# Kernel tuning notes

Hardware: AMD Instinct MI355X
Metric: run time of the kernel (lower is better)

Reference implementation:

```python
import jax, jax.numpy as jnp
import numpy as np

M = 256      # max_child_num
H = 256      # hidden_size
F = 256      # node feature_size (== H, required by original view())
T = 4        # edge_type_num
ITERS = 2    # num_dec_gnn_iterations
NSEM = 40    # Tree.num_sem


def setup_inputs() -> dict:
    key = jax.random.key(0)
    ks = jax.random.split(key, 18)

    def w(k, shape):
        fan_in = shape[-2] if len(shape) >= 2 else shape[-1]
        return jax.random.normal(k, shape, jnp.float32) / np.sqrt(fan_in)

    return {
        "parent_feature": jax.random.normal(ks[0], (1, F), jnp.float32),
        # mlp_parent: F -> H*M
        "W_parent": w(ks[1], (F, H * M)), "b_parent": jnp.zeros((H * M,), jnp.float32),
        # mlp_exists: H -> 1
        "W_exists": w(ks[2], (H, 1)), "b_exists": jnp.zeros((1,), jnp.float32),
        # mlp_edge_latent: 2H -> H
        "W_el": w(ks[3], (2 * H, H)), "b_el": jnp.zeros((H,), jnp.float32),
        # mlp_edge_exists[t]: H -> 1, stacked over T
        "W_ee": w(ks[4], (T, H)), "b_ee": jnp.zeros((T,), jnp.float32),
        # node_edge_op[i]: (3H + T) -> H, stacked over ITERS
        "W_ne": w(ks[5], (ITERS, 3 * H + T, H)), "b_ne": jnp.zeros((ITERS, H), jnp.float32),
        # mlp_child: H*(ITERS+1) -> H
        "W_child": w(ks[6], (H * (ITERS + 1), H)), "b_child": jnp.zeros((H,), jnp.float32),
        # mlp_sem: H -> NSEM
        "W_sem": w(ks[7], (H, NSEM)), "b_sem": jnp.zeros((NSEM,), jnp.float32),
        # mlp_child2: H -> F
        "W_child2": w(ks[8], (H, F)), "b_child2": jnp.zeros((F,), jnp.float32),
    }


def _forward(parent_feature, W_parent, b_parent, W_exists, b_exists,
             W_el, b_el, W_ee, b_ee, W_ne, b_ne,
             W_child, b_child, W_sem, b_sem, W_child2, b_child2):
    # parent -> per-child latent feats [M, H]
    pf = jax.nn.relu(parent_feature @ W_parent + b_parent)   # [1, M*H]
    child_feats = pf.reshape(M, H)

    child_exists_logits = child_feats @ W_exists + b_exists  # [M, 1]

    # pairwise edge latents [M, M, H]: relu(Linear(cat(feat_i, feat_j)))
    # split the 2H x H weight to avoid materializing the [M, M, 2H] concat
    W_el_i, W_el_j = W_el[:H], W_el[H:]
    edge_latents = jax.nn.relu(
        (child_feats @ W_el_i)[:, None, :] + (child_feats @ W_el_j)[None, :, :] + b_el
    )  # [M, M, H]

    # per-type edge existence logits [M, M, T]
    edge_exists_logits = jnp.einsum('mnh,th->mnt', edge_latents, W_ee) + b_ee

    # dynamic edge set (torch.nonzero) expressed as a dense mask over (i, j, t):
    # edge exists iff its logit > 0 and both endpoint nodes exist
    node_exists = child_exists_logits[:, 0] > 0                      # [M]
    edge_mask = (edge_exists_logits > 0) \
        & node_exists[:, None, None] & node_exists[None, :, None]    # [M, M, T]
    has_edge = jnp.any(edge_mask)

    cf = child_feats
    iter_feats = [cf]
    for i in range(ITERS):
        # node_edge_op input is cat([feat_i, feat_j, edge_latent, type_logit]);
        # split the (3H+T) x H weight into blocks to avoid the big concat.
        Wi, Wj = W_ne[i, :H], W_ne[i, H:2 * H]
        We, Wt = W_ne[i, 2 * H:3 * H], W_ne[i, 3 * H:]
        # type_logit is one-hot(t) * edge_exists_logits[i,j,t], so its matmul
        # contribution is logits[m,n,t] * Wt[t]
        pre = ((cf @ Wi)[:, None, None, :]
               + (cf @ Wj)[None, :, None, :]
               + jnp.einsum('mnh,hk->mnk', edge_latents, We)[:, :, None, :]
               + edge_exists_logits[..., None] * Wt[None, None, :, :]
               + b_ne[i])                                            # [M, M, T, H]
        msg = jax.nn.relu(pre)
        msg = jnp.where(edge_mask[..., None], msg, 0.0)
        # scatter_max over source node with zero-initialized out; msgs >= 0 so
        # masked-zero + max reproduces torch_scatter.scatter_max exactly
        new_cf = jnp.max(msg, axis=(1, 2))                           # [M, H]
        cf = jnp.where(has_edge, new_cf, cf)  # torch skips update if no edges
        iter_feats.append(cf)

    feats_cat = jnp.concatenate(iter_feats, axis=1)                  # [M, H*(ITERS+1)]
    hidden = jax.nn.relu(feats_cat @ W_child + b_child)              # [M, H]
    child_sem_logits = (hidden @ W_sem + b_sem).reshape(1, M, NSEM)
    out_child_feats = jax.nn.relu(hidden @ W_child2 + b_child2).reshape(1, M, F)
    return (out_child_feats,
            child_sem_logits,
            child_exists_logits.reshape(1, M, 1),
            edge_exists_logits.reshape(1, M, M, T))


def reference(parent_feature, W_parent, b_parent, W_exists, b_exists,
              W_el, b_el, W_ee, b_ee, W_ne, b_ne,
              W_child, b_child, W_sem, b_sem, W_child2, b_child2):
    return _forward(parent_feature, W_parent, b_parent, W_exists, b_exists,
                    W_el, b_el, W_ee, b_ee, W_ne, b_ne,
                    W_child, b_child, W_sem, b_sem, W_child2, b_child2)
```

## Files before the change

kernel.cpp:

```cpp
#include <hip/hip_runtime.h>
#include <hip/hip_bf16.h>

#define MMH 256
#define TT 4
#define NSEMN 40
#define HM 65536

using short8 = __attribute__((ext_vector_type(8))) short;
using f32x4  = __attribute__((ext_vector_type(4))) float;

__device__ __forceinline__ unsigned short f2bf(float x) {
  union { float f; unsigned int u; } v; v.f = x;
  unsigned int r = v.u + 0x7fffu + ((v.u >> 16) & 1u);
  return (unsigned short)(r >> 16);
}

__global__ __launch_bounds__(256) void k_parent(
    const float* __restrict__ pf, const float* __restrict__ Wp,
    const float* __restrict__ bp, float* __restrict__ cat) {
  int j = blockIdx.x * 256 + threadIdx.x;
  float acc = bp[j];
  #pragma unroll 8
  for (int f = 0; f < MMH; ++f) acc += pf[f] * Wp[(size_t)f * HM + j];
  int m = j >> 8, h = j & 255;
  cat[m * 768 + h] = fmaxf(acc, 0.0f);
}

__global__ __launch_bounds__(64) void k_cel(
    const float* __restrict__ cat, const float* __restrict__ Wex,
    const float* __restrict__ bex, float* __restrict__ cel,
    float* __restrict__ out_ex, int* __restrict__ flags) {
  int m = blockIdx.x, l = threadIdx.x;
  float s = 0.f;
  for (int h = l; h < MMH; h += 64) s += cat[m * 768 + h] * Wex[h];
  #pragma unroll
  for (int off = 32; off > 0; off >>= 1) s += __shfl_down(s, off);
  if (l == 0) { float v = s + bex[0]; cel[m] = v; out_ex[m] = v; }
  if (m == 0 && l == 0) flags[0] = 0;
}

__global__ __launch_bounds__(256) void k_gemm16(
    const float* __restrict__ A, int lda,
    const float* __restrict__ B0, const float* __restrict__ B1, int ldb,
    const float* __restrict__ bias,
    float* __restrict__ C0, float* __restrict__ C1, int ldc,
    int N2, int K2, int relu) {
  const float* B = blockIdx.z ? B1 : B0;
  float*       C = blockIdx.z ? C1 : C0;
  __shared__ float As[16][17], Bs[16][17];
  int tx = threadIdx.x, ty = threadIdx.y;
  int row = blockIdx.y * 16 + ty, col = blockIdx.x * 16 + tx;
  float acc = 0.f;
  for (int k0 = 0; k0 < K2; k0 += 16) {
    As[ty][tx] = A[row * lda + k0 + tx];
    Bs[ty][tx] = (col < N2) ? B[(k0 + ty) * ldb + col] : 0.f;
    __syncthreads();
    #pragma unroll
    for (int kk = 0; kk < 16; ++kk) acc += As[ty][kk] * Bs[kk][tx];
    __syncthreads();
  }
  if (col < N2) {
    if (bias) acc += bias[col];
    if (relu) acc = fmaxf(acc, 0.f);
    C[row * ldc + col] = acc;
  }
}

__global__ __launch_bounds__(256) void k_tr(
    const float* __restrict__ Wne, const float* __restrict__ Wee,
    unsigned short* __restrict__ WeTb, float* __restrict__ Wee4g) {
  int i = blockIdx.z;
  const float* We = Wne + (size_t)(i * 772 + 512) * 256;
  unsigned short* out = WeTb + i * 65536;
  __shared__ float t[32][33];
  int tx = threadIdx.x, ty = threadIdx.y;
  int h0 = blockIdx.y * 32, k0 = blockIdx.x * 32;
  #pragma unroll
  for (int j = 0; j < 4; ++j)
    t[ty + j * 8][tx] = We[(size_t)(h0 + ty + j * 8) * 256 + k0 + tx];
  __syncthreads();
  #pragma unroll
  for (int j = 0; j < 4; ++j) {
    int kl = ty + j * 8;
    out[((h0 >> 5) * 256 + k0 + kl) * 32 + tx] = f2bf(t[tx][kl]);
  }
  if (blockIdx.x == 0 && blockIdx.y == 0 && i == 0) {
    int t2 = ty * 32 + tx;
    float4 w;
    w.x = Wee[t2]; w.y = Wee[256 + t2]; w.z = Wee[512 + t2]; w.w = Wee[768 + t2];
    ((float4*)Wee4g)[t2] = w;
  }
}

#define XP 260
__global__ __launch_bounds__(256) void k_edge(
    const float* __restrict__ Xi, const float* __restrict__ Xj,
    const float* __restrict__ bel, const float* __restrict__ Wee4g,
    const float* __restrict__ bee, const float* __restrict__ cel,
    float* __restrict__ out_eel, int* __restrict__ flags) {
  __shared__ float XiS[16 * XP], XjS[16 * XP];
  __shared__ int anyEdge;
  int tid = threadIdx.x;
  int m0 = (blockIdx.x >> 4) * 16, n0 = (blockIdx.x & 15) * 16;
  if (tid == 0) anyEdge = 0;
  #pragma unroll
  for (int j = 0; j < 4; ++j) {
    int c = tid + 256 * j;
    int row = c >> 6, c4 = (c & 63) * 4;
    float4 v = *(const float4*)(Xi + (m0 + row) * 256 + c4);
    float4 b = *(const float4*)(bel + c4);
    v.x += b.x; v.y += b.y; v.z += b.z; v.w += b.w;
    *(float4*)&XiS[row * XP + c4] = v;
    *(float4*)&XjS[row * XP + c4] = *(const float4*)(Xj + (n0 + row) * 256 + c4);
  }
  __syncthreads();
  int tm = tid >> 4, tn = tid & 15;
  const float* xr = &XiS[tm * XP];
  const float* yr = &XjS[tn * XP];
  float4 s = {0.f, 0.f, 0.f, 0.f};
  for (int h = 0; h < 256; h += 8) {
    float4 a0 = *(const float4*)&xr[h], a1 = *(const float4*)&xr[h + 4];
    float4 b0 = *(const float4*)&yr[h], b1 = *(const float4*)&yr[h + 4];
    float e[8];
    e[0] = fmaxf(a0.x + b0.x, 0.f); e[1] = fmaxf(a0.y + b0.y, 0.f);
    e[2] = fmaxf(a0.z + b0.z, 0.f); e[3] = fmaxf(a0.w + b0.w, 0.f);
    e[4] = fmaxf(a1.x + b1.x, 0.f); e[5] = fmaxf(a1.y + b1.y, 0.f);
    e[6] = fmaxf(a1.z + b1.z, 0.f); e[7] = fmaxf(a1.w + b1.w, 0.f);
    #pragma unroll
    for (int q = 0; q < 8; ++q) {
      float4 w = ((const float4*)Wee4g)[h + q];
      s.x += e[q] * w.x; s.y += e[q] * w.y;
      s.z += e[q] * w.z; s.w += e[q] * w.w;
    }
  }
  int m = m0 + tm, n = n0 + tn;
  s.x += bee[0]; s.y += bee[1]; s.z += bee[2]; s.w += bee[3];
  ((float4*)out_eel)[m * 256 + n] = s;
  bool edge = (cel[m] > 0.f) && (cel[n] > 0.f) &&
              (s.x > 0.f || s.y > 0.f || s.z > 0.f || s.w > 0.f);
  if (__ballot(edge) != 0ull && (tid & 63) == 0) atomicOr(&anyEdge, 1);
  __syncthreads();
  if (tid == 0 && anyEdge) atomicOr(flags, 1);
}

__global__ __launch_bounds__(256) void k_zero(float* __restrict__ p) {
  p[blockIdx.x * 256 + threadIdx.x] = 0.f;
}

#define ELP 56
__global__ __launch_bounds__(256) void k_iter(
    const float* __restrict__ Xi, const float* __restrict__ Xj,
    const float* __restrict__ bel, const unsigned short* __restrict__ WeTb,
    const float* __restrict__ Ai, const float* __restrict__ Bj,
    const float* __restrict__ Wt, const float* __restrict__ bne,
    const float* __restrict__ eel, const float* __restrict__ cel,
    float* __restrict__ newcf) {
  __shared__ unsigned short ELs[64 * ELP];
  __shared__ unsigned short WesT[256 * ELP];
  int tid = threadIdx.x;
  int w = tid >> 6, lane = tid & 63;
  int m0 = (blockIdx.x >> 4) * 4, n0 = (blockIdx.x & 15) * 16;
  f32x4 acc[4][4] = {};

  for (int h0 = 0; h0 < MMH; h0 += 32) {
    {
      int row = tid & 63, g = tid >> 6;
      int mI = m0 + (row >> 4), nI = n0 + (row & 15);
      const float4* xip = (const float4*)(Xi + mI * MMH + h0 + g * 8);
      const float4* xjp = (const float4*)(Xj + nI * MMH + h0 + g * 8);
      const float4* bp  = (const float4*)(bel + h0 + g * 8);
      float4 x0 = xip[0], x1 = xip[1];
      float4 y0 = xjp[0], y1 = xjp[1];
      float4 c0 = bp[0],  c1 = bp[1];
      short8 v;
      v[0] = (short)f2bf(fmaxf(x0.x + y0.x + c0.x, 0.f));
      v[1] = (short)f2bf(fmaxf(x0.y + y0.y + c0.y, 0.f));
      v[2] = (short)f2bf(fmaxf(x0.z + y0.z + c0.z, 0.f));
      v[3] = (short)f2bf(fmaxf(x0.w + y0.w + c0.w, 0.f));
      v[4] = (short)f2bf(fmaxf(x1.x + y1.x + c1.x, 0.f));
      v[5] = (short)f2bf(fmaxf(x1.y + y1.y + c1.y, 0.f));
      v[6] = (short)f2bf(fmaxf(x1.z + y1.z + c1.z, 0.f));
      v[7] = (short)f2bf(fmaxf(x1.w + y1.w + c1.w, 0.f));
      *(short8*)&ELs[row * ELP + g * 8] = v;
    }
    {
      const unsigned short* WeT = WeTb + (h0 >> 5) * 8192;
      #pragma unroll
      for (int j = 0; j < 4; ++j) {
        int g = tid + 256 * j;
        short8 v = *(const short8*)(WeT + g * 8);
        *(short8*)&WesT[(g >> 2) * ELP + (g & 3) * 8] = v;
      }
    }
    __syncthreads();
    short8 af[4], bf[4];
    #pragma unroll
    for (int rt = 0; rt < 4; ++rt)
      af[rt] = *(const short8*)&ELs[(rt * 16 + (lane & 15)) * ELP + (lane >> 4) * 8];
    #pragma unroll
    for (int ct = 0; ct < 4; ++ct)
      bf[ct] = *(const short8*)&WesT[(w * 64 + ct * 16 + (lane & 15)) * ELP + (lane >> 4) * 8];
    #pragma unroll
    for (int rt = 0; rt < 4; ++rt)
      #pragma unroll
      for (int ct = 0; ct < 4; ++ct)
        acc[rt][ct] = __builtin_amdgcn_mfma_f32_16x16x32_bf16(af[rt], bf[ct], acc[rt][ct], 0, 0, 0);
    __syncthreads();
  }

  int col = lane & 15, grp = lane >> 4;
  #pragma unroll
  for (int rt = 0; rt < 4; ++rt) {
    int m = m0 + rt;
    bool nem = cel[m] > 0.f;
    float4 e4[4]; bool nen[4];
    #pragma unroll
    for (int r = 0; r < 4; ++r) {
      int n = n0 + grp * 4 + r;
      e4[r] = ((const float4*)eel)[m * 256 + n];
      nen[r] = cel[n] > 0.f;
    }
    #pragma unroll
    for (int ct = 0; ct < 4; ++ct) {
      int k = w * 64 + ct * 16 + col;
      float basek = Ai[m * MMH + k] + bne[k];
      float wt0 = Wt[0 * MMH + k], wt1 = Wt[1 * MMH + k];
      float wt2 = Wt[2 * MMH + k], wt3 = Wt[3 * MMH + k];
      float vmax = 0.f;
      #pragma unroll
      for (int r = 0; r < 4; ++r) {
        int n = n0 + grp * 4 + r;
        float base = acc[rt][ct][r] + basek + Bj[n * MMH + k];
        if (nem && nen[r]) {
          if (e4[r].x > 0.f) vmax = fmaxf(vmax, base + e4[r].x * wt0);
          if (e4[r].y > 0.f) vmax = fmaxf(vmax, base + e4[r].y * wt1);
          if (e4[r].z > 0.f) vmax = fmaxf(vmax, base + e4[r].z * wt2);
          if (e4[r].w > 0.f) vmax = fmaxf(vmax, base + e4[r].w * wt3);
        }
      }
      vmax = fmaxf(vmax, __shfl_xor(vmax, 16));
      vmax = fmaxf(vmax, __shfl_xor(vmax, 32));
      if (grp == 0 && vmax > 0.f)
        atomicMax((unsigned int*)&newcf[m * MMH + k], __float_as_uint(vmax));
    }
  }
}

__global__ __launch_bounds__(256) void k_select(
    const int* __restrict__ flags, float* __restrict__ newcf,
    float* __restrict__ cat, int iter) {
  int idx = blockIdx.x * 256 + threadIdx.x;
  int m = idx >> 8, k = idx & 255;
  float prev = cat[m * 768 + iter * 256 + k];
  float v = flags[0] ? newcf[idx] : prev;
  cat[m * 768 + (iter + 1) * 256 + k] = v;
  newcf[idx] = 0.f;
}

extern "C" void kernel_launch(void* const* d_in, const int* in_sizes, int n_in,
                              void* d_out, int out_size, void* d_ws, size_t ws_size,
                              hipStream_t stream) {
  const float* pf   = (const float*)d_in[0];
  const float* Wp   = (const float*)d_in[1];
  const float* bp   = (const float*)d_in[2];
  const float* Wex  = (const float*)d_in[3];
  const float* bex  = (const float*)d_in[4];
  const float* Wel  = (const float*)d_in[5];
  const float* bel  = (const float*)d_in[6];
  const float* Wee  = (const float*)d_in[7];
  const float* bee  = (const float*)d_in[8];
  const float* Wne  = (const float*)d_in[9];
  const float* bne  = (const float*)d_in[10];
  const float* Wch  = (const float*)d_in[11];
  const float* bch  = (const float*)d_in[12];
  const float* Wsem = (const float*)d_in[13];
  const float* bsem = (const float*)d_in[14];
  const float* Wch2 = (const float*)d_in[15];
  const float* bch2 = (const float*)d_in[16];
  float* out = (float*)d_out;
  float* ws  = (float*)d_ws;

  float* cat    = ws;
  float* Xi     = ws + 196608;
  float* Xj     = Xi + 65536;
  float* Ai     = Xj + 65536;
  float* Bj     = Ai + 65536;
  float* newcf  = Bj + 65536;
  float* hidden = newcf + 65536;
  float* cel    = hidden + 65536;
  int*   flags  = (int*)(cel + 256);
  float* Wee4g  = cel + 512;
  unsigned short* WeTb = (unsigned short*)(Wee4g + 1024);

  float* out_cf  = out;
  float* out_sem = out + 65536;
  float* out_ex  = out + 75776;
  float* out_eel = out + 76032;

  dim3 b16(16, 16);
  k_parent<<<256, 256, 0, stream>>>(pf, Wp, bp, cat);
  k_cel<<<256, 64, 0, stream>>>(cat, Wex, bex, cel, out_ex, flags);
  k_tr<<<dim3(8, 8, 2), dim3(32, 8), 0, stream>>>(Wne, Wee, WeTb, Wee4g);
  k_gemm16<<<dim3(16, 16, 2), b16, 0, stream>>>(cat, 768, Wel, Wel + 65536, 256,
                                                nullptr, Xi, Xj, 256, 256, 256, 0);
  k_edge<<<256, 256, 0, stream>>>(Xi, Xj, bel, Wee4g, bee, cel, out_eel, flags);
  k_zero<<<256, 256, 0, stream>>>(newcf);
  for (int i = 0; i < 2; ++i) {
    const float* cfi = cat + i * 256;
    const float* Wi  = Wne + (size_t)(i * 772 + 0)   * 256;
    const float* Wj  = Wne + (size_t)(i * 772 + 256) * 256;
    const float* Wt  = Wne + (size_t)(i * 772 + 768) * 256;
    const float* bnei = bne + i * 256;
    k_gemm16<<<dim3(16, 16, 2), b16, 0, stream>>>(cfi, 768, Wi, Wj, 256,
                                                  nullptr, Ai, Bj, 256, 256, 256, 0);
    k_iter<<<1024, 256, 0, stream>>>(Xi, Xj, bel, WeTb + i * 65536,
                                     Ai, Bj, Wt, bnei, out_eel, cel, newcf);
    k_select<<<256, 256, 0, stream>>>(flags, newcf, cat, i);
  }
  k_gemm16<<<dim3(16, 16, 1), b16, 0, stream>>>(cat, 768, Wch, nullptr, 256, bch,
                                                hidden, nullptr, 256, 256, 768, 1);
  k_gemm16<<<dim3(3, 16, 1), b16, 0, stream>>>(hidden, 256, Wsem, nullptr, 40, bsem,
                                               out_sem, nullptr, 40, NSEMN, 256, 0);
  k_gemm16<<<dim3(16, 16, 1), b16, 0, stream>>>(hidden, 256, Wch2, nullptr, 256, bch2,
                                                out_cf, nullptr, 256, 256, 256, 1);
}
```

Measured before the change: 350.2 us.

## Materialize bf16 edge-latent tensor once and stream it into iteration MFMAs

k_edge now writes the relu'd pairwise edge latents as a bf16 [M,M,H] tensor (32 MB) into workspace when it is large enough. A new k_iter_fast kernel loads MFMA operands straight from that tensor and the transposed weights, with no LDS staging and no recomputation, in both GNN iterations. The first iteration's Ai/Bj GEMM is folded into the Xi/Xj GEMM launch through a 4-way z-dimension. The trade is one large extra global write plus two large reads in place of recomputing relu(Xi+Xj+b) per iteration, and the fast path only runs if the workspace holds it.

```diff
diff --git a/kernel.cpp b/kernel.cpp
--- a/kernel.cpp
+++ b/kernel.cpp
@@ -41,12 +41,15 @@
 
 __global__ __launch_bounds__(256) void k_gemm16(
     const float* __restrict__ A, int lda,
-    const float* __restrict__ B0, const float* __restrict__ B1, int ldb,
+    const float* __restrict__ B0, const float* __restrict__ B1,
+    const float* __restrict__ B2, const float* __restrict__ B3, int ldb,
     const float* __restrict__ bias,
-    float* __restrict__ C0, float* __restrict__ C1, int ldc,
+    float* __restrict__ C0, float* __restrict__ C1,
+    float* __restrict__ C2, float* __restrict__ C3, int ldc,
     int N2, int K2, int relu) {
-  const float* B = blockIdx.z ? B1 : B0;
-  float*       C = blockIdx.z ? C1 : C0;
+  int z = blockIdx.z;
+  const float* B = (z == 0) ? B0 : (z == 1) ? B1 : (z == 2) ? B2 : B3;
+  float*       C = (z == 0) ? C0 : (z == 1) ? C1 : (z == 2) ? C2 : C3;
   __shared__ float As[16][17], Bs[16][17];
   int tx = threadIdx.x, ty = threadIdx.y;
   int row = blockIdx.y * 16 + ty, col = blockIdx.x * 16 + tx;
@@ -97,7 +100,8 @@
     const float* __restrict__ Xi, const float* __restrict__ Xj,
     const float* __restrict__ bel, const float* __restrict__ Wee4g,
     const float* __restrict__ bee, const float* __restrict__ cel,
-    float* __restrict__ out_eel, int* __restrict__ flags) {
+    float* __restrict__ out_eel, int* __restrict__ flags,
+    unsigned short* __restrict__ ELmat) {
   __shared__ float XiS[16 * XP], XjS[16 * XP];
   __shared__ int anyEdge;
   int tid = threadIdx.x;
@@ -115,6 +119,8 @@
   }
   __syncthreads();
   int tm = tid >> 4, tn = tid & 15;
+  int m = m0 + tm, n = n0 + tn;
+  unsigned short* elp = ELmat ? ELmat + (size_t)(m * 256 + n) * 256 : nullptr;
   const float* xr = &XiS[tm * XP];
   const float* yr = &XjS[tn * XP];
   float4 s = {0.f, 0.f, 0.f, 0.f};
@@ -126,6 +132,12 @@
     e[2] = fmaxf(a0.z + b0.z, 0.f); e[3] = fmaxf(a0.w + b0.w, 0.f);
     e[4] = fmaxf(a1.x + b1.x, 0.f); e[5] = fmaxf(a1.y + b1.y, 0.f);
     e[6] = fmaxf(a1.z + b1.z, 0.f); e[7] = fmaxf(a1.w + b1.w, 0.f);
+    if (elp) {
+      short8 vv;
+      #pragma unroll
+      for (int q = 0; q < 8; ++q) vv[q] = (short)f2bf(e[q]);
+      *(short8*)&elp[h] = vv;
+    }
     #pragma unroll
     for (int q = 0; q < 8; ++q) {
       float4 w = ((const float4*)Wee4g)[h + q];
@@ -133,7 +145,6 @@
       s.z += e[q] * w.z; s.w += e[q] * w.w;
     }
   }
-  int m = m0 + tm, n = n0 + tn;
   s.x += bee[0]; s.y += bee[1]; s.z += bee[2]; s.w += bee[3];
   ((float4*)out_eel)[m * 256 + n] = s;
   bool edge = (cel[m] > 0.f) && (cel[n] > 0.f) &&
@@ -147,8 +158,84 @@
   p[blockIdx.x * 256 + threadIdx.x] = 0.f;
 }
 
+__device__ __forceinline__ void iter_epilogue(
+    f32x4 (&acc)[4][4], int m0, int n0, int w, int lane,
+    const float* __restrict__ Ai, const float* __restrict__ Bj,
+    const float* __restrict__ Wt, const float* __restrict__ bne,
+    const float* __restrict__ eel, const float* __restrict__ cel,
+    float* __restrict__ newcf) {
+  int col = lane & 15, grp = lane >> 4;
+  #pragma unroll
+  for (int rt = 0; rt < 4; ++rt) {
+    int m = m0 + rt;
+    bool nem = cel[m] > 0.f;
+    float4 e4[4]; bool nen[4];
+    #pragma unroll
+    for (int r = 0; r < 4; ++r) {
+      int n = n0 + grp * 4 + r;
+      e4[r] = ((const float4*)eel)[m * 256 + n];
+      nen[r] = cel[n] > 0.f;
+    }
+    #pragma unroll
+    for (int ct = 0; ct < 4; ++ct) {
+      int k = w * 64 + ct * 16 + col;
+      float basek = Ai[m * MMH + k] + bne[k];
+      float wt0 = Wt[0 * MMH + k], wt1 = Wt[1 * MMH + k];
+      float wt2 = Wt[2 * MMH + k], wt3 = Wt[3 * MMH + k];
+      float vmax = 0.f;
+      #pragma unroll
+      for (int r = 0; r < 4; ++r) {
+        int n = n0 + grp * 4 + r;
+        float base = acc[rt][ct][r] + basek + Bj[n * MMH + k];
+        if (nem && nen[r]) {
+          if (e4[r].x > 0.f) vmax = fmaxf(vmax, base + e4[r].x * wt0);
+          if (e4[r].y > 0.f) vmax = fmaxf(vmax, base + e4[r].y * wt1);
+          if (e4[r].z > 0.f) vmax = fmaxf(vmax, base + e4[r].z * wt2);
+          if (e4[r].w > 0.f) vmax = fmaxf(vmax, base + e4[r].w * wt3);
+        }
+      }
+      vmax = fmaxf(vmax, __shfl_xor(vmax, 16));
+      vmax = fmaxf(vmax, __shfl_xor(vmax, 32));
+      if (grp == 0 && vmax > 0.f)
+        atomicMax((unsigned int*)&newcf[m * MMH + k], __float_as_uint(vmax));
+    }
+  }
+}
+
+__global__ __launch_bounds__(256) void k_iter_fast(
+    const unsigned short* __restrict__ ELmat,
+    const unsigned short* __restrict__ WeTb,
+    const float* __restrict__ Ai, const float* __restrict__ Bj,
+    const float* __restrict__ Wt, const float* __restrict__ bne,
+    const float* __restrict__ eel, const float* __restrict__ cel,
+    float* __restrict__ newcf) {
+  int tid = threadIdx.x;
+  int w = tid >> 6, lane = tid & 63;
+  int m0 = (blockIdx.x >> 4) * 4, n0 = (blockIdx.x & 15) * 16;
+  int kl = lane & 15, colh = (lane >> 4) * 8;
+  f32x4 acc[4][4] = {};
+  const unsigned short* elbase = ELmat + ((size_t)(m0 * 256 + n0 + kl)) * 256 + colh;
+  const unsigned short* webase = WeTb + (size_t)(w * 64 + kl) * 32 + colh;
+  for (int s = 0; s < 8; ++s) {
+    int h0 = s * 32;
+    short8 af[4], bf[4];
+    #pragma unroll
+    for (int rt = 0; rt < 4; ++rt)
+      af[rt] = *(const short8*)(elbase + (size_t)rt * 65536 + h0);
+    #pragma unroll
+    for (int ct = 0; ct < 4; ++ct)
+      bf[ct] = *(const short8*)(webase + (size_t)(s * 256 + ct * 16) * 32);
+    #pragma unroll
+    for (int rt = 0; rt < 4; ++rt)
+      #pragma unroll
+      for (int ct = 0; ct < 4; ++ct)
+        acc[rt][ct] = __builtin_amdgcn_mfma_f32_16x16x32_bf16(af[rt], bf[ct], acc[rt][ct], 0, 0, 0);
+  }
+  iter_epilogue(acc, m0, n0, w, lane, Ai, Bj, Wt, bne, eel, cel, newcf);
+}
+
 #define ELP 56
-__global__ __launch_bounds__(256) void k_iter(
+__global__ __launch_bounds__(256) void k_iter_lds(
     const float* __restrict__ Xi, const float* __restrict__ Xj,
     const float* __restrict__ bel, const unsigned short* __restrict__ WeTb,
     const float* __restrict__ Ai, const float* __restrict__ Bj,
@@ -161,7 +248,6 @@
   int w = tid >> 6, lane = tid & 63;
   int m0 = (blockIdx.x >> 4) * 4, n0 = (blockIdx.x & 15) * 16;
   f32x4 acc[4][4] = {};
-
   for (int h0 = 0; h0 < MMH; h0 += 32) {
     {
       int row = tid & 63, g = tid >> 6;
@@ -207,43 +293,7 @@
         acc[rt][ct] = __builtin_amdgcn_mfma_f32_16x16x32_bf16(af[rt], bf[ct], acc[rt][ct], 0, 0, 0);
     __syncthreads();
   }
-
-  int col = lane & 15, grp = lane >> 4;
-  #pragma unroll
-  for (int rt = 0; rt < 4; ++rt) {
-    int m = m0 + rt;
-    bool nem = cel[m] > 0.f;
-    float4 e4[4]; bool nen[4];
-    #pragma unroll
-    for (int r = 0; r < 4; ++r) {
-      int n = n0 + grp * 4 + r;
-      e4[r] = ((const float4*)eel)[m * 256 + n];
-      nen[r] = cel[n] > 0.f;
-    }
-    #pragma unroll
-    for (int ct = 0; ct < 4; ++ct) {
-      int k = w * 64 + ct * 16 + col;
-      float basek = Ai[m * MMH + k] + bne[k];
-      float wt0 = Wt[0 * MMH + k], wt1 = Wt[1 * MMH + k];
-      float wt2 = Wt[2 * MMH + k], wt3 = Wt[3 * MMH + k];
-      float vmax = 0.f;
-      #pragma unroll
-      for (int r = 0; r < 4; ++r) {
-        int n = n0 + grp * 4 + r;
-        float base = acc[rt][ct][r] + basek + Bj[n * MMH + k];
-        if (nem && nen[r]) {
-          if (e4[r].x > 0.f) vmax = fmaxf(vmax, base + e4[r].x * wt0);
-          if (e4[r].y > 0.f) vmax = fmaxf(vmax, base + e4[r].y * wt1);
-          if (e4[r].z > 0.f) vmax = fmaxf(vmax, base + e4[r].z * wt2);
-          if (e4[r].w > 0.f) vmax = fmaxf(vmax, base + e4[r].w * wt3);
-        }
-      }
-      vmax = fmaxf(vmax, __shfl_xor(vmax, 16));
-      vmax = fmaxf(vmax, __shfl_xor(vmax, 32));
-      if (grp == 0 && vmax > 0.f)
-        atomicMax((unsigned int*)&newcf[m * MMH + k], __float_as_uint(vmax));
-    }
-  }
+  iter_epilogue(acc, m0, n0, w, lane, Ai, Bj, Wt, bne, eel, cel, newcf);
 }
 
 __global__ __launch_bounds__(256) void k_select(
@@ -290,37 +340,54 @@
   float* cel    = hidden + 65536;
   int*   flags  = (int*)(cel + 256);
   float* Wee4g  = cel + 512;
-  unsigned short* WeTb = (unsigned short*)(Wee4g + 1024);
+  unsigned short* WeTb  = (unsigned short*)(Wee4g + 1024);
+  unsigned short* ELmat = WeTb + 131072;
+  size_t need = (size_t)((char*)(ELmat + (size_t)65536 * 256) - (char*)ws);
+  bool fast = ws_size >= need;
 
   float* out_cf  = out;
   float* out_sem = out + 65536;
   float* out_ex  = out + 75776;
   float* out_eel = out + 76032;
 
+  const float* Wi0 = Wne + (size_t)(0 * 772 + 0)   * 256;
+  const float* Wj0 = Wne + (size_t)(0 * 772 + 256) * 256;
+  const float* Wi1 = Wne + (size_t)(1 * 772 + 0)   * 256;
+  const float* Wj1 = Wne + (size_t)(1 * 772 + 256) * 256;
+
   dim3 b16(16, 16);
   k_parent<<<256, 256, 0, stream>>>(pf, Wp, bp, cat);
   k_cel<<<256, 64, 0, stream>>>(cat, Wex, bex, cel, out_ex, flags);
   k_tr<<<dim3(8, 8, 2), dim3(32, 8), 0, stream>>>(Wne, Wee, WeTb, Wee4g);
-  k_gemm16<<<dim3(16, 16, 2), b16, 0, stream>>>(cat, 768, Wel, Wel + 65536, 256,
-                                                nullptr, Xi, Xj, 256, 256, 256, 0);
-  k_edge<<<256, 256, 0, stream>>>(Xi, Xj, bel, Wee4g, bee, cel, out_eel, flags);
   k_zero<<<256, 256, 0, stream>>>(newcf);
+  k_gemm16<<<dim3(16, 16, 4), b16, 0, stream>>>(cat, 768,
+      Wel, Wel + 65536, Wi0, Wj0, 256, nullptr,
+      Xi, Xj, Ai, Bj, 256, 256, 256, 0);
+  k_edge<<<256, 256, 0, stream>>>(Xi, Xj, bel, Wee4g, bee, cel, out_eel, flags,
+                                  fast ? ELmat : nullptr);
   for (int i = 0; i < 2; ++i) {
-    const float* cfi = cat + i * 256;
-    const float* Wi  = Wne + (size_t)(i * 772 + 0)   * 256;
-    const float* Wj  = Wne + (size_t)(i * 772 + 256) * 256;
     const float* Wt  = Wne + (size_t)(i * 772 + 768) * 256;
     const float* bnei = bne + i * 256;
-    k_gemm16<<<dim3(16, 16, 2), b16, 0, stream>>>(cfi, 768, Wi, Wj, 256,
-                                                  nullptr, Ai, Bj, 256, 256, 256, 0);
-    k_iter<<<1024, 256, 0, stream>>>(Xi, Xj, bel, WeTb + i * 65536,
-                                     Ai, Bj, Wt, bnei, out_eel, cel, newcf);
+    if (i == 1) {
+      k_gemm16<<<dim3(16, 16, 2), b16, 0, stream>>>(cat + 256, 768,
+          Wi1, Wj1, nullptr, nullptr, 256, nullptr,
+          Ai, Bj, nullptr, nullptr, 256, 256, 256, 0);
+    }
+    if (fast)
+      k_iter_fast<<<1024, 256, 0, stream>>>(ELmat, WeTb + i * 65536,
+                                            Ai, Bj, Wt, bnei, out_eel, cel, newcf);
+    else
+      k_iter_lds<<<1024, 256, 0, stream>>>(Xi, Xj, bel, WeTb + i * 65536,
+                                           Ai, Bj, Wt, bnei, out_eel, cel, newcf);
     k_select<<<256, 256, 0, stream>>>(flags, newcf, cat, i);
   }
-  k_gemm16<<<dim3(16, 16, 1), b16, 0, stream>>>(cat, 768, Wch, nullptr, 256, bch,
-                                                hidden, nullptr, 256, 256, 768, 1);
-  k_gemm16<<<dim3(3, 16, 1), b16, 0, stream>>>(hidden, 256, Wsem, nullptr, 40, bsem,
-                                               out_sem, nullptr, 40, NSEMN, 256, 0);
-  k_gemm16<<<dim3(16, 16, 1), b16, 0, stream>>>(hidden, 256, Wch2, nullptr, 256, bch2,
-                                                out_cf, nullptr, 256, 256, 256, 1);
-}
+  k_gemm16<<<dim3(16, 16, 1), b16, 0, stream>>>(cat, 768,
+      Wch, nullptr, nullptr, nullptr, 256, bch,
+      hidden, nullptr, nullptr, nullptr, 256, 256, 768, 1);
+  k_gemm16<<<dim3(3, 16, 1), b16, 0, stream>>>(hidden, 256,
+      Wsem, nullptr, nullptr, nullptr, 40, bsem,
+      out_sem, nullptr, nullptr, nullptr, 40, NSEMN, 256, 0);
+  k_gemm16<<<dim3(16, 16, 1), b16, 0, stream>>>(hidden, 256,
+      Wch2, nullptr, nullptr, nullptr, 256, bch2,
+      out_cf, nullptr, nullptr, nullptr, 256, 256, 256, 1);
+}
```

Result: slower. 369.1 us (+5.4%).
